# Performance work log

Hardware: AMD Instinct MI355X
Metric: run time of the kernel (lower is better)

## Reference

```python
import jax, jax.numpy as jnp
import numpy as np

HEAD_DIM = 128
N_HEADS = 64
N_KV = 8
N_REP = 8
DIM = 5120
HID = 25600
EPS_LN = 1e-5
EPS_QK = 1e-6
MAX_SEQ = 1024
BSZ = 32


def rmsnorm(x, w, eps):
    xf = x.astype(jnp.float32)
    n = xf * jax.lax.rsqrt(jnp.mean(xf * xf, axis=-1, keepdims=True) + eps)
    return n.astype(x.dtype) * w


def rope(x, cos, sin):
    # x: [b, s, h, d]; cos/sin: [s, d//2]. Complex rotation on (even, odd) pairs.
    xr = x[..., 0::2]
    xi = x[..., 1::2]
    c = cos[None, :, None, :]
    s = sin[None, :, None, :]
    o_r = xr * c - xi * s
    o_i = xr * s + xi * c
    return jnp.stack([o_r, o_i], axis=-1).reshape(x.shape)


def setup_inputs() -> dict:
    key = jax.random.key(0)
    ks = jax.random.split(key, 12)
    seqlen = 1
    start_pos = MAX_SEQ - seqlen
    x = jax.random.normal(ks[0], (BSZ, seqlen, DIM), jnp.float32)
    pos = np.arange(start_pos, start_pos + seqlen)
    inv = 1.0 / (10000.0 ** (np.arange(0, HEAD_DIM, 2, dtype=np.float64) / HEAD_DIM))
    ang = pos[:, None] * inv[None, :]
    freqs_cos = jnp.asarray(np.cos(ang), jnp.float32)
    freqs_sin = jnp.asarray(np.sin(ang), jnp.float32)
    mask = jnp.zeros((1, 1, seqlen, start_pos + seqlen), jnp.float32)
    cache_k = jax.random.normal(ks[1], (BSZ, MAX_SEQ, N_KV, HEAD_DIM), jnp.float32)
    cache_v = jax.random.normal(ks[2], (BSZ, MAX_SEQ, N_KV, HEAD_DIM), jnp.float32)
    s = 0.02
    wq = jax.random.normal(ks[3], (N_HEADS * HEAD_DIM, DIM), jnp.float32) * s
    wk = jax.random.normal(ks[4], (N_KV * HEAD_DIM, DIM), jnp.float32) * s
    wv = jax.random.normal(ks[5], (N_KV * HEAD_DIM, DIM), jnp.float32) * s
    wo = jax.random.normal(ks[6], (DIM, N_HEADS * HEAD_DIM), jnp.float32) * s
    w1 = jax.random.normal(ks[7], (HID, DIM), jnp.float32) * s
    w2 = jax.random.normal(ks[8], (DIM, HID), jnp.float32) * s
    w3 = jax.random.normal(ks[9], (HID, DIM), jnp.float32) * s
    attn_norm_w = jnp.ones((DIM,), jnp.float32)
    ffn_norm_w = jnp.ones((DIM,), jnp.float32)
    q_norm_w = jnp.ones((HEAD_DIM,), jnp.float32)
    k_norm_w = jnp.ones((HEAD_DIM,), jnp.float32)
    return dict(x=x, start_pos=start_pos, freqs_cos=freqs_cos, freqs_sin=freqs_sin,
                mask=mask, cache_k=cache_k, cache_v=cache_v,
                wq=wq, wk=wk, wv=wv, wo=wo, w1=w1, w2=w2, w3=w3,
                attn_norm_w=attn_norm_w, ffn_norm_w=ffn_norm_w,
                q_norm_w=q_norm_w, k_norm_w=k_norm_w)


def reference(x, start_pos, freqs_cos, freqs_sin, mask, cache_k, cache_v,
              wq, wk, wv, wo, w1, w2, w3,
              attn_norm_w, ffn_norm_w, q_norm_w, k_norm_w):
    bsz, seqlen, _ = x.shape
    # --- attention branch ---
    an = rmsnorm(x, attn_norm_w, EPS_LN)
    xq = (an @ wq.T).reshape(bsz, seqlen, N_HEADS, HEAD_DIM)
    xk = (an @ wk.T).reshape(bsz, seqlen, N_KV, HEAD_DIM)
    xv = (an @ wv.T).reshape(bsz, seqlen, N_KV, HEAD_DIM)
    xq = rmsnorm(xq, q_norm_w, EPS_QK)
    xk = rmsnorm(xk, k_norm_w, EPS_QK)
    xq = rope(xq, freqs_cos, freqs_sin)
    xk = rope(xk, freqs_cos, freqs_sin)
    # KV-cache write (start_pos is a static Python int)
    cache_k = cache_k.at[:bsz, start_pos:start_pos + seqlen].set(xk)
    cache_v = cache_v.at[:bsz, start_pos:start_pos + seqlen].set(xv)
    L = start_pos + seqlen
    keys = cache_k[:bsz, :L]      # [b, L, g, d]
    values = cache_v[:bsz, :L]    # [b, L, g, d]
    # GQA via grouped einsum (math-equivalent to repeat_kv then matmul)
    qg = xq.reshape(bsz, seqlen, N_KV, N_REP, HEAD_DIM)  # head = g*N_REP + r
    scores = jnp.einsum('bqgrd,blgd->bgrql', qg, keys) / np.sqrt(HEAD_DIM).astype(np.float32)
    scores = scores + mask[:, :, None, :, :]  # [1,1,1,q,L] broadcast
    probs = jax.nn.softmax(scores.astype(jnp.float32), axis=-1).astype(xq.dtype)
    attn = jnp.einsum('bgrql,blgd->bqgrd', probs, values)
    attn = attn.reshape(bsz, seqlen, N_HEADS * HEAD_DIM)
    h = x + attn @ wo.T
    # --- SwiGLU FFN branch ---
    fn = rmsnorm(h, ffn_norm_w, EPS_LN)
    ff = (jax.nn.silu(fn @ w1.T) * (fn @ w3.T)) @ w2.T
    return h + ff
```

## Files before the change

kernel.cpp:

```cpp
#include <hip/hip_runtime.h>
#include <math.h>

#define DIM   5120
#define QD    8192
#define KVD   1024
#define NQKV  10240
#define NH    64
#define NKV   8
#define HD    128
#define HID   25600
#define SEQL  1024
#define BSZ   32
#define NSEG  8

typedef __attribute__((ext_vector_type(8))) short short8;
typedef __attribute__((ext_vector_type(4))) float f32x4;
typedef __attribute__((ext_vector_type(4))) unsigned short us4;

__device__ __forceinline__ unsigned short f2bf(float f) {
  unsigned u = __builtin_bit_cast(unsigned, f);
  unsigned r = u + 0x7fffu + ((u >> 16) & 1u);
  return (unsigned short)(r >> 16);
}
__device__ __forceinline__ float bf2f(unsigned short b) {
  return __builtin_bit_cast(float, (unsigned)b << 16);
}
__device__ __forceinline__ float fma4(float4 a, float4 b, float acc) {
  acc = fmaf(a.x, b.x, acc);
  acc = fmaf(a.y, b.y, acc);
  acc = fmaf(a.z, b.z, acc);
  acc = fmaf(a.w, b.w, acc);
  return acc;
}

__global__ __launch_bounds__(256) void rmsnorm_bf_kernel(
    const float* __restrict__ x, const float* __restrict__ w,
    unsigned short* __restrict__ out, float eps) {
  int b = blockIdx.x, t = threadIdx.x;
  const float4* xp = reinterpret_cast<const float4*>(x + (size_t)b * DIM);
  const float4* wp = reinterpret_cast<const float4*>(w);
  us4* op = reinterpret_cast<us4*>(out + (size_t)b * DIM);
  float4 v[5];
  float ss = 0.f;
#pragma unroll
  for (int j = 0; j < 5; ++j) {
    v[j] = xp[t + j * 256];
    ss = fma4(v[j], v[j], ss);
  }
#pragma unroll
  for (int m = 1; m < 64; m <<= 1) ss += __shfl_xor(ss, m);
  __shared__ float red[4];
  if ((t & 63) == 0) red[t >> 6] = ss;
  __syncthreads();
  float sc = rsqrtf((red[0] + red[1] + red[2] + red[3]) * (1.f / DIM) + eps);
#pragma unroll
  for (int j = 0; j < 5; ++j) {
    float4 wv = wp[t + j * 256];
    us4 o;
    o[0] = f2bf(v[j].x * sc * wv.x);
    o[1] = f2bf(v[j].y * sc * wv.y);
    o[2] = f2bf(v[j].z * sc * wv.z);
    o[3] = f2bf(v[j].w * sc * wv.w);
    op[t + j * 256] = o;
  }
}

#define LDSW 136
template <int OUT_BF>
__device__ __forceinline__ void gemm_body(
    const unsigned short* __restrict__ Abf, const float* __restrict__ W,
    void* __restrict__ outp, int K, int k0, int kLen,
    int n0row, int n0col, int Nstride, int t) {
  __shared__ unsigned short lw[32 * LDSW];
  const int lane = t & 63;
  const int r = lane & 15, kg = lane >> 4;
  const int wid = t >> 6;
  const int rgrp = wid & 1, bgrp = wid >> 1;
  const int srow = t >> 5;
  const int skf  = (t & 31) * 4;
  const float* wbase = W + (size_t)n0row * K + k0 + skf;
  const unsigned short* abase =
      Abf + (size_t)(bgrp * 16 + r) * K + k0 + kg * 8;
  f32x4 acc = {0.f, 0.f, 0.f, 0.f};
  const int nsteps = kLen >> 7;
  float4 pre[4];
#pragma unroll
  for (int j = 0; j < 4; ++j)
    pre[j] = *reinterpret_cast<const float4*>(wbase + (size_t)(j * 8 + srow) * K);
  for (int s = 0; s < nsteps; ++s) {
    __syncthreads();
#pragma unroll
    for (int j = 0; j < 4; ++j) {
      us4 o;
      o[0] = f2bf(pre[j].x);
      o[1] = f2bf(pre[j].y);
      o[2] = f2bf(pre[j].z);
      o[3] = f2bf(pre[j].w);
      *reinterpret_cast<us4*>(&lw[(j * 8 + srow) * LDSW + skf]) = o;
    }
    if (s + 1 < nsteps) {
      const float* wb2 = wbase + (size_t)(s + 1) * 128;
#pragma unroll
      for (int j = 0; j < 4; ++j)
        pre[j] = *reinterpret_cast<const float4*>(wb2 + (size_t)(j * 8 + srow) * K);
    }
    __syncthreads();
    const unsigned short* ab = abase + (size_t)s * 128;
#pragma unroll
    for (int c = 0; c < 4; ++c) {
      short8 wf = *reinterpret_cast<const short8*>(
          &lw[(rgrp * 16 + r) * LDSW + c * 32 + kg * 8]);
      short8 af = *reinterpret_cast<const short8*>(ab + c * 32);
      acc = __builtin_amdgcn_mfma_f32_16x16x32_bf16(wf, af, acc, 0, 0, 0);
    }
  }
  int ncol = n0col + rgrp * 16 + kg * 4;
  int brow = bgrp * 16 + r;
#pragma unroll
  for (int j = 0; j < 4; ++j) {
    if (OUT_BF) {
      ((unsigned short*)outp)[(size_t)brow * Nstride + ncol + j] = f2bf(acc[j]);
    } else {
      ((float*)outp)[(size_t)brow * Nstride + ncol + j] = acc[j];
    }
  }
}

__global__ __launch_bounds__(256) void qkv_gemm_kernel(
    const unsigned short* __restrict__ an_bf, const float* __restrict__ wq,
    const float* __restrict__ wk, const float* __restrict__ wv,
    float* __restrict__ part) {
  int n = blockIdx.x * 32;
  const float* W;
  int n0row;
  if (n < QD)            { W = wq; n0row = n; }
  else if (n < QD + KVD) { W = wk; n0row = n - QD; }
  else                   { W = wv; n0row = n - QD - KVD; }
  float* outp = part + (size_t)blockIdx.y * BSZ * NQKV;
  gemm_body<0>(an_bf, W, outp, DIM, blockIdx.y * 1280, 1280, n0row, n, NQKV,
               threadIdx.x);
}

__global__ __launch_bounds__(256) void wo_gemm_kernel(
    const unsigned short* __restrict__ ao_bf, const float* __restrict__ wo,
    float* __restrict__ part) {
  int n = blockIdx.x * 32;
  float* outp = part + (size_t)blockIdx.y * BSZ * DIM;
  gemm_body<0>(ao_bf, wo, outp, QD, blockIdx.y * 1024, 1024, n, n, DIM,
               threadIdx.x);
}

__global__ __launch_bounds__(256) void w13_gemm_kernel(
    const unsigned short* __restrict__ fn_bf, const float* __restrict__ w1,
    const float* __restrict__ w3, unsigned short* __restrict__ g13) {
  int n = blockIdx.x * 32;
  const float* W;
  int n0row;
  if (n < HID) { W = w1; n0row = n; }
  else         { W = w3; n0row = n - HID; }
  gemm_body<1>(fn_bf, W, g13, DIM, 0, DIM, n0row, n, 2 * HID, threadIdx.x);
}

__global__ __launch_bounds__(256) void w2_gemm_kernel(
    const unsigned short* __restrict__ gg_bf, const float* __restrict__ w2,
    float* __restrict__ part) {
  int n = blockIdx.x * 32;
  float* outp = part + (size_t)blockIdx.y * BSZ * DIM;
  gemm_body<0>(gg_bf, w2, outp, HID, blockIdx.y * 3200, 3200, n, n, DIM,
               threadIdx.x);
}

__global__ __launch_bounds__(64) void qkv_finish_kernel(
    const float* __restrict__ part, const float* __restrict__ qw,
    const float* __restrict__ kw, const float* __restrict__ fcos,
    const float* __restrict__ fsin, float* __restrict__ xqkv) {
  int h = blockIdx.x, b = blockIdx.y, j = threadIdx.x;
  int base;
  const float* w = nullptr;
  int dorope = 1;
  if (h < NH)            { base = h * HD; w = qw; }
  else if (h < NH + NKV) { base = QD + (h - NH) * HD; w = kw; }
  else                   { base = QD + KVD + (h - NH - NKV) * HD; dorope = 0; }
  size_t off = (size_t)b * NQKV + base;
  float s0 = 0.f, s1 = 0.f;
#pragma unroll
  for (int g = 0; g < 4; ++g) {
    const float* p = part + (size_t)g * BSZ * NQKV + off;
    s0 += p[2 * j];
    s1 += p[2 * j + 1];
  }
  if (dorope) {
    float ss = s0 * s0 + s1 * s1;
#pragma unroll
    for (int m = 1; m < 64; m <<= 1) ss += __shfl_xor(ss, m);
    float sc = rsqrtf(ss * (1.f / HD) + 1e-6f);
    float n0 = s0 * sc * w[2 * j];
    float n1 = s1 * sc * w[2 * j + 1];
    float c = fcos[j], s = fsin[j];
    xqkv[off + 2 * j]     = n0 * c - n1 * s;
    xqkv[off + 2 * j + 1] = n0 * s + n1 * c;
  } else {
    xqkv[off + 2 * j]     = s0;
    xqkv[off + 2 * j + 1] = s1;
  }
}

__global__ __launch_bounds__(256) void wo_finish_kernel(
    const float* __restrict__ part, const float* __restrict__ x,
    const float* __restrict__ fw, float* __restrict__ h,
    unsigned short* __restrict__ fn_bf, float eps) {
  int b = blockIdx.x, t = threadIdx.x;
  const float4* xp = reinterpret_cast<const float4*>(x + (size_t)b * DIM);
  const float4* wp = reinterpret_cast<const float4*>(fw);
  float4* hp = reinterpret_cast<float4*>(h + (size_t)b * DIM);
  us4* fp = reinterpret_cast<us4*>(fn_bf + (size_t)b * DIM);
  float4 v[5];
  float ss = 0.f;
#pragma unroll
  for (int j = 0; j < 5; ++j) {
    int idx = t + j * 256;
    float4 s = xp[idx];
#pragma unroll
    for (int g = 0; g < 8; ++g) {
      float4 p = reinterpret_cast<const float4*>(
          part + (size_t)g * BSZ * DIM + (size_t)b * DIM)[idx];
      s.x += p.x; s.y += p.y; s.z += p.z; s.w += p.w;
    }
    v[j] = s;
    ss = fma4(s, s, ss);
    hp[idx] = s;
  }
#pragma unroll
  for (int m = 1; m < 64; m <<= 1) ss += __shfl_xor(ss, m);
  __shared__ float red[4];
  if ((t & 63) == 0) red[t >> 6] = ss;
  __syncthreads();
  float sc = rsqrtf((red[0] + red[1] + red[2] + red[3]) * (1.f / DIM) + eps);
#pragma unroll
  for (int j = 0; j < 5; ++j) {
    float4 wv = wp[t + j * 256];
    us4 o;
    o[0] = f2bf(v[j].x * sc * wv.x);
    o[1] = f2bf(v[j].y * sc * wv.y);
    o[2] = f2bf(v[j].z * sc * wv.z);
    o[3] = f2bf(v[j].w * sc * wv.w);
    fp[t + j * 256] = o;
  }
}

template <int SEGS>
__global__ __launch_bounds__(256) void combine_kernel(
    const float* __restrict__ part, const float* __restrict__ resid,
    float* __restrict__ out, int total) {
  int i = blockIdx.x * 256 + threadIdx.x;
  if (i >= total) return;
  float s = 0.f;
#pragma unroll
  for (int g = 0; g < SEGS; ++g) s += part[(size_t)g * total + i];
  if (resid) s += resid[i];
  out[i] = s;
}

__global__ __launch_bounds__(256) void attn_kernel(
    const float* __restrict__ xqkv, const float* __restrict__ ck,
    const float* __restrict__ cv, float* __restrict__ pacc,
    float* __restrict__ pml) {
  int g = blockIdx.x, b = blockIdx.y, z = blockIdx.z, t = threadIdx.x;
  __shared__ float qs[8][128];
  __shared__ float tk[128][33];
  __shared__ float tv[32][132];
  __shared__ float st[8][32];
  __shared__ float m_s[8], sum_s[8], fac_s[8];
  const float* qbase = xqkv + (size_t)b * NQKV;
  for (int i = t; i < 8 * 128; i += 256)
    qs[i >> 7][i & 127] = qbase[(g * 8 + (i >> 7)) * HD + (i & 127)];
  if (t < 8) { m_s[t] = -1e30f; sum_s[t] = 0.f; }
  int r = t >> 5, d5 = t & 31;
  float4 acc = make_float4(0.f, 0.f, 0.f, 0.f);
  for (int ti = 0; ti < 1024 / NSEG / 32; ++ti) {
    int l0 = z * (1024 / NSEG) + ti * 32;
    __syncthreads();
#pragma unroll
    for (int jj = 0; jj < 4; ++jj) {
      int i = t + jj * 256;
      int l = i >> 5, d4 = i & 31;
      int gl = l0 + l;
      float4 kv, vv;
      if (gl == 1023) {
        kv = *reinterpret_cast<const float4*>(qbase + QD + g * HD + d4 * 4);
        vv = *reinterpret_cast<const float4*>(qbase + QD + KVD + g * HD + d4 * 4);
      } else {
        size_t base = (((size_t)b * SEQL + gl) * NKV + g) * HD + d4 * 4;
        kv = *reinterpret_cast<const float4*>(ck + base);
        vv = *reinterpret_cast<const float4*>(cv + base);
      }
      tk[d4 * 4 + 0][l] = kv.x;
      tk[d4 * 4 + 1][l] = kv.y;
      tk[d4 * 4 + 2][l] = kv.z;
      tk[d4 * 4 + 3][l] = kv.w;
      *reinterpret_cast<float4*>(&tv[l][d4 * 4]) = vv;
    }
    __syncthreads();
    {
      int l = t & 31, rr = t >> 5;
      float s = 0.f;
#pragma unroll 8
      for (int d = 0; d < 128; ++d) s = fmaf(qs[rr][d], tk[d][l], s);
      st[rr][l] = s * 0.08838834764831845f;
    }
    __syncthreads();
    {
      float sv = st[r][d5];
      float tm = sv;
#pragma unroll
      for (int m = 1; m < 32; m <<= 1) tm = fmaxf(tm, __shfl_xor(tm, m));
      float mo = m_s[r];
      float mn = fmaxf(mo, tm);
      float fac = __expf(mo - mn);
      float e = __expf(sv - mn);
      st[r][d5] = e;
      float ps = e;
#pragma unroll
      for (int m = 1; m < 32; m <<= 1) ps += __shfl_xor(ps, m);
      if (d5 == 0) {
        sum_s[r] = sum_s[r] * fac + ps;
        m_s[r] = mn;
        fac_s[r] = fac;
      }
    }
    __syncthreads();
    {
      float fac = fac_s[r];
      acc.x *= fac; acc.y *= fac; acc.z *= fac; acc.w *= fac;
#pragma unroll 4
      for (int l = 0; l < 32; ++l) {
        float p = st[r][l];
        float4 vv = *reinterpret_cast<const float4*>(&tv[l][d5 * 4]);
        acc.x = fmaf(p, vv.x, acc.x);
        acc.y = fmaf(p, vv.y, acc.y);
        acc.z = fmaf(p, vv.z, acc.z);
        acc.w = fmaf(p, vv.w, acc.w);
      }
    }
  }
  size_t idx = ((size_t)b * NH + g * 8 + r) * NSEG + z;
  *reinterpret_cast<float4*>(pacc + idx * HD + d5 * 4) = acc;
  if (d5 == 0) {
    pml[idx * 2]     = m_s[r];
    pml[idx * 2 + 1] = sum_s[r];
  }
}

__global__ __launch_bounds__(128) void attn_combine_kernel(
    const float* __restrict__ pacc, const float* __restrict__ pml,
    unsigned short* __restrict__ ao_bf) {
  int h = blockIdx.x, b = blockIdx.y, d = threadIdx.x;
  size_t base = ((size_t)b * NH + h) * NSEG;
  float M = -1e30f;
#pragma unroll
  for (int s = 0; s < NSEG; ++s) M = fmaxf(M, pml[(base + s) * 2]);
  float L = 0.f, o = 0.f;
#pragma unroll
  for (int s = 0; s < NSEG; ++s) {
    float w = __expf(pml[(base + s) * 2] - M);
    L += pml[(base + s) * 2 + 1] * w;
    o += pacc[(base + s) * HD + d] * w;
  }
  ao_bf[((size_t)b * NH + h) * HD + d] = f2bf(o / L);
}

__global__ __launch_bounds__(256) void silu_mul_bf_kernel(
    const unsigned short* __restrict__ g13, unsigned short* __restrict__ gg) {
  int j = blockIdx.x * 256 + threadIdx.x;
  int b = blockIdx.y;
  float a = bf2f(g13[(size_t)b * 2 * HID + j]);
  float c = bf2f(g13[(size_t)b * 2 * HID + HID + j]);
  gg[(size_t)b * HID + j] = f2bf((a / (1.f + __expf(-a))) * c);
}

extern "C" void kernel_launch(void* const* d_in, const int* in_sizes, int n_in,
                              void* d_out, int out_size, void* d_ws, size_t ws_size,
                              hipStream_t stream) {
  const float* x    = (const float*)d_in[0];
  const float* fcos = (const float*)d_in[2];
  const float* fsin = (const float*)d_in[3];
  const float* ck   = (const float*)d_in[5];
  const float* cv   = (const float*)d_in[6];
  const float* wq   = (const float*)d_in[7];
  const float* wk   = (const float*)d_in[8];
  const float* wv   = (const float*)d_in[9];
  const float* wo   = (const float*)d_in[10];
  const float* w1   = (const float*)d_in[11];
  const float* w2   = (const float*)d_in[12];
  const float* w3   = (const float*)d_in[13];
  const float* anw  = (const float*)d_in[14];
  const float* fnw  = (const float*)d_in[15];
  const float* qnw  = (const float*)d_in[16];
  const float* knw  = (const float*)d_in[17];
  float* out = (float*)d_out;

  char* wsb = (char*)d_ws;
  float* scratch = (float*)wsb;                 wsb += 16 * 1024 * 1024;
  unsigned short* an_bf  = (unsigned short*)wsb; wsb += (size_t)BSZ * DIM * 2;
  unsigned short* ao_bf  = (unsigned short*)wsb; wsb += (size_t)BSZ * QD * 2;
  unsigned short* g13_bf = (unsigned short*)wsb; wsb += (size_t)BSZ * 2 * HID * 2;
  unsigned short* gg_bf  = (unsigned short*)wsb; wsb += (size_t)BSZ * HID * 2;
  unsigned short* fn_bf  = (unsigned short*)wsb; wsb += (size_t)BSZ * DIM * 2;
  float*          xqkv   = (float*)wsb;          wsb += (size_t)BSZ * NQKV * 4;
  float*          h      = (float*)wsb;          wsb += (size_t)BSZ * DIM * 4;
  float* pacc = scratch;
  float* pml  = scratch + (size_t)BSZ * NH * NSEG * HD;

  rmsnorm_bf_kernel<<<BSZ, 256, 0, stream>>>(x, anw, an_bf, 1e-5f);
  qkv_gemm_kernel<<<dim3(NQKV / 32, 4), 256, 0, stream>>>(an_bf, wq, wk, wv, scratch);
  qkv_finish_kernel<<<dim3(NH + 2 * NKV, BSZ), 64, 0, stream>>>(
      scratch, qnw, knw, fcos, fsin, xqkv);
  attn_kernel<<<dim3(NKV, BSZ, NSEG), 256, 0, stream>>>(xqkv, ck, cv, pacc, pml);
  attn_combine_kernel<<<dim3(NH, BSZ), 128, 0, stream>>>(pacc, pml, ao_bf);
  wo_gemm_kernel<<<dim3(DIM / 32, 8), 256, 0, stream>>>(ao_bf, wo, scratch);
  wo_finish_kernel<<<BSZ, 256, 0, stream>>>(scratch, x, fnw, h, fn_bf, 1e-5f);
  w13_gemm_kernel<<<dim3(2 * HID / 32, 1), 256, 0, stream>>>(fn_bf, w1, w3, g13_bf);
  silu_mul_bf_kernel<<<dim3(HID / 256, BSZ), 256, 0, stream>>>(g13_bf, gg_bf);
  w2_gemm_kernel<<<dim3(DIM / 32, 8), 256, 0, stream>>>(gg_bf, w2, scratch);
  combine_kernel<8><<<(BSZ * DIM + 255) / 256, 256, 0, stream>>>(
      scratch, h, out, BSZ * DIM);
}
```

Baseline: 533.0 us.

## Widen GEMM k-tile, add split-K to FFN GEMMs, use nontemporal weight loads

The shared GEMM body now stages 256-wide k-slices per step, with each wave loading whole row segments, and fetches weights and KV cache through nontemporal loads. The w1/w3 GEMM gains a 4-way split-K that writes fp32 partials, which a new fused silu-combine kernel sums. The w2 GEMM moves from an 8-way to a 20-way split. The aim is more blocks and more in-flight memory requests so the weight-bandwidth-bound decode GEMMs keep HBM busy, at the cost of extra partial-sum traffic and a larger scratch buffer.

```diff
diff --git a/kernel.cpp b/kernel.cpp
--- a/kernel.cpp
+++ b/kernel.cpp
@@ -65,7 +65,7 @@
   }
 }
 
-#define LDSW 136
+#define LDSW 264
 template <int OUT_BF>
 __device__ __forceinline__ void gemm_body(
     const unsigned short* __restrict__ Abf, const float* __restrict__ W,
@@ -73,41 +73,40 @@
     int n0row, int n0col, int Nstride, int t) {
   __shared__ unsigned short lw[32 * LDSW];
   const int lane = t & 63;
+  const int wv = t >> 6;
   const int r = lane & 15, kg = lane >> 4;
-  const int wid = t >> 6;
-  const int rgrp = wid & 1, bgrp = wid >> 1;
-  const int srow = t >> 5;
-  const int skf  = (t & 31) * 4;
-  const float* wbase = W + (size_t)n0row * K + k0 + skf;
-  const unsigned short* abase =
-      Abf + (size_t)(bgrp * 16 + r) * K + k0 + kg * 8;
+  const int rgrp = wv & 1, bgrp = wv >> 1;
+  const float* wbase = W + (size_t)n0row * K + k0 + lane * 4;
+  const unsigned short* abase = Abf + (size_t)(bgrp * 16 + r) * K + k0 + kg * 8;
   f32x4 acc = {0.f, 0.f, 0.f, 0.f};
-  const int nsteps = kLen >> 7;
-  float4 pre[4];
-#pragma unroll
-  for (int j = 0; j < 4; ++j)
-    pre[j] = *reinterpret_cast<const float4*>(wbase + (size_t)(j * 8 + srow) * K);
+  const int nsteps = kLen >> 8;
+  f32x4 pre[8];
+#pragma unroll
+  for (int j = 0; j < 8; ++j)
+    pre[j] = __builtin_nontemporal_load(
+        reinterpret_cast<const f32x4*>(wbase + (size_t)(j * 4 + wv) * K));
   for (int s = 0; s < nsteps; ++s) {
     __syncthreads();
 #pragma unroll
-    for (int j = 0; j < 4; ++j) {
+    for (int j = 0; j < 8; ++j) {
       us4 o;
-      o[0] = f2bf(pre[j].x);
-      o[1] = f2bf(pre[j].y);
-      o[2] = f2bf(pre[j].z);
-      o[3] = f2bf(pre[j].w);
-      *reinterpret_cast<us4*>(&lw[(j * 8 + srow) * LDSW + skf]) = o;
+      o[0] = f2bf(pre[j][0]);
+      o[1] = f2bf(pre[j][1]);
+      o[2] = f2bf(pre[j][2]);
+      o[3] = f2bf(pre[j][3]);
+      *reinterpret_cast<us4*>(&lw[(j * 4 + wv) * LDSW + lane * 4]) = o;
     }
     if (s + 1 < nsteps) {
-      const float* wb2 = wbase + (size_t)(s + 1) * 128;
-#pragma unroll
-      for (int j = 0; j < 4; ++j)
-        pre[j] = *reinterpret_cast<const float4*>(wb2 + (size_t)(j * 8 + srow) * K);
-    }
-    __syncthreads();
-    const unsigned short* ab = abase + (size_t)s * 128;
-#pragma unroll
-    for (int c = 0; c < 4; ++c) {
+      const float* wb2 = wbase + (size_t)(s + 1) * 256;
+#pragma unroll
+      for (int j = 0; j < 8; ++j)
+        pre[j] = __builtin_nontemporal_load(
+            reinterpret_cast<const f32x4*>(wb2 + (size_t)(j * 4 + wv) * K));
+    }
+    __syncthreads();
+    const unsigned short* ab = abase + (size_t)s * 256;
+#pragma unroll
+    for (int c = 0; c < 8; ++c) {
       short8 wf = *reinterpret_cast<const short8*>(
           &lw[(rgrp * 16 + r) * LDSW + c * 32 + kg * 8]);
       short8 af = *reinterpret_cast<const short8*>(ab + c * 32);
@@ -152,13 +151,15 @@
 
 __global__ __launch_bounds__(256) void w13_gemm_kernel(
     const unsigned short* __restrict__ fn_bf, const float* __restrict__ w1,
-    const float* __restrict__ w3, unsigned short* __restrict__ g13) {
+    const float* __restrict__ w3, float* __restrict__ part) {
   int n = blockIdx.x * 32;
   const float* W;
   int n0row;
   if (n < HID) { W = w1; n0row = n; }
   else         { W = w3; n0row = n - HID; }
-  gemm_body<1>(fn_bf, W, g13, DIM, 0, DIM, n0row, n, 2 * HID, threadIdx.x);
+  float* outp = part + (size_t)blockIdx.y * BSZ * 2 * HID;
+  gemm_body<0>(fn_bf, W, outp, DIM, blockIdx.y * 1280, 1280, n0row, n,
+               2 * HID, threadIdx.x);
 }
 
 __global__ __launch_bounds__(256) void w2_gemm_kernel(
@@ -166,7 +167,7 @@
     float* __restrict__ part) {
   int n = blockIdx.x * 32;
   float* outp = part + (size_t)blockIdx.y * BSZ * DIM;
-  gemm_body<0>(gg_bf, w2, outp, HID, blockIdx.y * 3200, 3200, n, n, DIM,
+  gemm_body<0>(gg_bf, w2, outp, HID, blockIdx.y * 1280, 1280, n, n, DIM,
                threadIdx.x);
 }
 
@@ -246,6 +247,21 @@
     o[3] = f2bf(v[j].w * sc * wv.w);
     fp[t + j * 256] = o;
   }
+}
+
+__global__ __launch_bounds__(256) void silu_combine_kernel(
+    const float* __restrict__ part, unsigned short* __restrict__ gg) {
+  int j = blockIdx.x * 256 + threadIdx.x;
+  int b = blockIdx.y;
+  size_t row = (size_t)b * 2 * HID;
+  float a = 0.f, c = 0.f;
+#pragma unroll
+  for (int g = 0; g < 4; ++g) {
+    const float* p = part + (size_t)g * BSZ * 2 * HID + row;
+    a += p[j];
+    c += p[j + HID];
+  }
+  gg[(size_t)b * HID + j] = f2bf((a / (1.f + __expf(-a))) * c);
 }
 
 template <int SEGS>
@@ -285,20 +301,20 @@
       int i = t + jj * 256;
       int l = i >> 5, d4 = i & 31;
       int gl = l0 + l;
-      float4 kv, vv;
+      f32x4 kv, vv;
       if (gl == 1023) {
-        kv = *reinterpret_cast<const float4*>(qbase + QD + g * HD + d4 * 4);
-        vv = *reinterpret_cast<const float4*>(qbase + QD + KVD + g * HD + d4 * 4);
+        kv = *reinterpret_cast<const f32x4*>(qbase + QD + g * HD + d4 * 4);
+        vv = *reinterpret_cast<const f32x4*>(qbase + QD + KVD + g * HD + d4 * 4);
       } else {
         size_t base = (((size_t)b * SEQL + gl) * NKV + g) * HD + d4 * 4;
-        kv = *reinterpret_cast<const float4*>(ck + base);
-        vv = *reinterpret_cast<const float4*>(cv + base);
+        kv = __builtin_nontemporal_load(reinterpret_cast<const f32x4*>(ck + base));
+        vv = __builtin_nontemporal_load(reinterpret_cast<const f32x4*>(cv + base));
       }
-      tk[d4 * 4 + 0][l] = kv.x;
-      tk[d4 * 4 + 1][l] = kv.y;
-      tk[d4 * 4 + 2][l] = kv.z;
-      tk[d4 * 4 + 3][l] = kv.w;
-      *reinterpret_cast<float4*>(&tv[l][d4 * 4]) = vv;
+      tk[d4 * 4 + 0][l] = kv[0];
+      tk[d4 * 4 + 1][l] = kv[1];
+      tk[d4 * 4 + 2][l] = kv[2];
+      tk[d4 * 4 + 3][l] = kv[3];
+      *reinterpret_cast<f32x4*>(&tv[l][d4 * 4]) = vv;
     }
     __syncthreads();
     {
@@ -367,15 +383,6 @@
     o += pacc[(base + s) * HD + d] * w;
   }
   ao_bf[((size_t)b * NH + h) * HD + d] = f2bf(o / L);
-}
-
-__global__ __launch_bounds__(256) void silu_mul_bf_kernel(
-    const unsigned short* __restrict__ g13, unsigned short* __restrict__ gg) {
-  int j = blockIdx.x * 256 + threadIdx.x;
-  int b = blockIdx.y;
-  float a = bf2f(g13[(size_t)b * 2 * HID + j]);
-  float c = bf2f(g13[(size_t)b * 2 * HID + HID + j]);
-  gg[(size_t)b * HID + j] = f2bf((a / (1.f + __expf(-a))) * c);
 }
 
 extern "C" void kernel_launch(void* const* d_in, const int* in_sizes, int n_in,
@@ -400,10 +407,9 @@
   float* out = (float*)d_out;
 
   char* wsb = (char*)d_ws;
-  float* scratch = (float*)wsb;                 wsb += 16 * 1024 * 1024;
+  float* scratch = (float*)wsb;                  wsb += 28 * 1024 * 1024;
   unsigned short* an_bf  = (unsigned short*)wsb; wsb += (size_t)BSZ * DIM * 2;
   unsigned short* ao_bf  = (unsigned short*)wsb; wsb += (size_t)BSZ * QD * 2;
-  unsigned short* g13_bf = (unsigned short*)wsb; wsb += (size_t)BSZ * 2 * HID * 2;
   unsigned short* gg_bf  = (unsigned short*)wsb; wsb += (size_t)BSZ * HID * 2;
   unsigned short* fn_bf  = (unsigned short*)wsb; wsb += (size_t)BSZ * DIM * 2;
   float*          xqkv   = (float*)wsb;          wsb += (size_t)BSZ * NQKV * 4;
@@ -419,9 +425,9 @@
   attn_combine_kernel<<<dim3(NH, BSZ), 128, 0, stream>>>(pacc, pml, ao_bf);
   wo_gemm_kernel<<<dim3(DIM / 32, 8), 256, 0, stream>>>(ao_bf, wo, scratch);
   wo_finish_kernel<<<BSZ, 256, 0, stream>>>(scratch, x, fnw, h, fn_bf, 1e-5f);
-  w13_gemm_kernel<<<dim3(2 * HID / 32, 1), 256, 0, stream>>>(fn_bf, w1, w3, g13_bf);
-  silu_mul_bf_kernel<<<dim3(HID / 256, BSZ), 256, 0, stream>>>(g13_bf, gg_bf);
-  w2_gemm_kernel<<<dim3(DIM / 32, 8), 256, 0, stream>>>(gg_bf, w2, scratch);
-  combine_kernel<8><<<(BSZ * DIM + 255) / 256, 256, 0, stream>>>(
+  w13_gemm_kernel<<<dim3(2 * HID / 32, 4), 256, 0, stream>>>(fn_bf, w1, w3, scratch);
+  silu_combine_kernel<<<dim3(HID / 256, BSZ), 256, 0, stream>>>(scratch, gg_bf);
+  w2_gemm_kernel<<<dim3(DIM / 32, 20), 256, 0, stream>>>(gg_bf, w2, scratch);
+  combine_kernel<20><<<(BSZ * DIM + 255) / 256, 256, 0, stream>>>(
       scratch, h, out, BSZ * DIM);
 }
```

New measurement: 539.8 us. Within noise of the previous version (+1.3%).
